# Kernel optimization log

Hardware: AMD Instinct MI355X
Metric: run time of the kernel (lower is better)

## Reference

```python
import jax, jax.numpy as jnp
import numpy as np
from jax import lax

RADIUS = 9
EPS = 1e-5
CLAMP = 100.0


def _local_corr(a_pad, b):
    """For each shift (i,j) in [0,RADIUS)^2: sum_c a_pad[:, :, i:i+h, j:j+w] * b.
    a_pad: [n,c,h+2R,w+2R] replicate-padded, b: [n,c,h,w] -> [n, R*R, h, w].
    Matches the torch loop ordering idx = i*RADIUS + j."""
    n, c, h, w = b.shape
    offs = jnp.arange(RADIUS)

    def one(i, j):
        win = lax.dynamic_slice(a_pad, (0, 0, i, j), (n, c, h, w))
        return jnp.sum(win * b, axis=1)  # [n,h,w]

    corr = jax.vmap(lambda i: jax.vmap(lambda j: one(i, j))(offs))(offs)  # [R,R,n,h,w]
    return corr.reshape(RADIUS * RADIUS, n, h, w).transpose(1, 0, 2, 3)  # [n,R*R,h,w]


def setup_inputs() -> dict:
    key = jax.random.key(0)
    k1, k2 = jax.random.split(key)
    n, c, h, w = 2, 64, 128, 192
    img = jax.random.normal(k1, (n, c, h, w), dtype=jnp.float32)
    img_map = jax.random.normal(k2, (n, c, h, w), dtype=jnp.float32)
    return {"img": img, "img_map": img_map}


def reference(img, img_map):
    # channel-wise L2 normalization (torch.norm(p=2, dim=1))
    norm_img = jnp.linalg.norm(img, axis=1, keepdims=True)
    norm_map = jnp.linalg.norm(img_map, axis=1, keepdims=True)
    img_scaled = img / (norm_img + EPS)        # torch mutates img in-place to this
    map_scaled = img_map / (norm_map + EPS)    # img_map itself NOT mutated (div, not div_)
    img_clamped = jnp.clip(img_scaled, -CLAMP, CLAMP)
    map_clamped = jnp.clip(map_scaled, -CLAMP, CLAMP)

    pad = ((0, 0), (0, 0), (RADIUS, RADIUS), (RADIUS, RADIUS))
    map_clamped_pad = jnp.pad(map_clamped, pad, mode='edge')  # F.pad 'replicate'
    map_orig_pad = jnp.pad(img_map, pad, mode='edge')

    # out_cos = 1 - <clamped normalized img, shifted clamped normalized map>
    out_cos = 1.0 - _local_corr(map_clamped_pad, img_clamped)
    # out_diss uses the in-place-normalized (UNclamped) img and the ORIGINAL img_map
    out_diss = _local_corr(map_orig_pad, img_scaled)
    return out_cos, out_diss
```

## Files before the change

kernel.cpp:

```cpp
#include <hip/hip_runtime.h>
#include <math.h>

namespace {
constexpr int RADIUS = 9;
constexpr float EPSV = 1e-5f;
constexpr int N_ = 2, C_ = 64, H_ = 128, W_ = 192;
constexpr int HW  = H_ * W_;
constexpr int CHW = C_ * HW;
constexpr size_t OUT1 = (size_t)N_ * 81 * HW;

constexpr int XT = 64, YT = 4;
constexpr int NT = 256;
constexpr int NW = 4;
constexpr int ROUNDS = 16;
constexpr int MROWS = 4;
constexpr int NCH = 19;
constexpr int MCOLS = 76;
constexpr int MAP_SLOTS = MROWS * NCH;
constexpr int OFF_INVM = 5 * 256 * 4;
constexpr int LDS_F = OFF_INVM + MROWS * MCOLS;
}

__global__ __launch_bounds__(64)
void norms_kernel(const float* __restrict__ mp,
                  float* __restrict__ invM) {
    __shared__ float4 sM[8][8];
    const int tid = threadIdx.x;
    const int cg = tid >> 3;
    const int s  = tid & 7;
    const int q4 = blockIdx.x * 8 + s;
    const int n = q4 / (HW / 4);
    const int pix = (q4 - n * (HW / 4)) * 4;
    const float* pm = mp + (size_t)n * CHW + pix;

    float4 sm = {0.f, 0.f, 0.f, 0.f};
#pragma unroll
    for (int cc = 0; cc < 8; ++cc) {
        float4 b = *(const float4*)(pm + (size_t)(cg * 8 + cc) * HW);
        sm.x = fmaf(b.x, b.x, sm.x); sm.y = fmaf(b.y, b.y, sm.y);
        sm.z = fmaf(b.z, b.z, sm.z); sm.w = fmaf(b.w, b.w, sm.w);
    }
    sM[cg][s] = sm;
    __syncthreads();
    if (tid < 8) {
        float4 b = sM[0][tid];
#pragma unroll
        for (int g = 1; g < 8; ++g) {
            float4 v = sM[g][tid];
            b.x += v.x; b.y += v.y; b.z += v.z; b.w += v.w;
        }
        float4 vm;
        vm.x = 1.f / (sqrtf(b.x) + EPSV); vm.y = 1.f / (sqrtf(b.y) + EPSV);
        vm.z = 1.f / (sqrtf(b.z) + EPSV); vm.w = 1.f / (sqrtf(b.w) + EPSV);
        *(float4*)(invM + (size_t)n * HW + pix) = vm;
    }
}

__global__ __launch_bounds__(NT)
void corr_kernel(const float* __restrict__ img,
                 const float* __restrict__ mp,
                 const float* __restrict__ invMg,
                 float* __restrict__ out) {
    __shared__ float smem[LDS_F];

    const int bz = blockIdx.z;
    const int n    = bz / RADIUS;
    const int iOff = bz - n * RADIUS;
    const int y0 = blockIdx.y * YT;
    const int x0 = blockIdx.x * XT;
    const int tid = threadIdx.x;
    const int w    = tid >> 6;
    const int lane = tid & 63;
    const int ty = lane >> 4;
    const int xc = lane & 15;
    const int ch0 = w * 16;

    const float* imgN = img + (size_t)n * CHW;
    const float* mapN = mp  + (size_t)n * CHW;

    if (tid < MAP_SLOTS) {
        int r = tid / NCH, k = tid - r * NCH;
        int gy = min(max(y0 + iOff - RADIUS + r, 0), H_ - 1);
        int gxs = x0 - 12 + 4 * k;
        const float* src = invMg + n * HW + (size_t)gy * W_;
        float4 v;
        if (gxs >= 0) v = *(const float4*)(src + gxs);
        else { float s0 = src[0]; v.x = s0; v.y = s0; v.z = s0; v.w = s0; }
        *(float4*)&smem[OFF_INVM + r * MCOLS + 4 * k] = v;
    }

    const int gy = min(max(y0 + ty + iOff - RADIUS, 0), H_ - 1);
    const float* rowp = mapN + (size_t)ch0 * HW + (size_t)gy * W_;
    bool bc[4]; const float* pd[4];
#pragma unroll
    for (int d = 0; d < 4; ++d) {
        int gx = x0 + 4 * xc - 12 + 4 * d;
        bc[d] = (gx < 0);
        pd[d] = rowp + (gx < 0 ? 0 : gx);
    }
    const float* pI = imgN + (size_t)ch0 * HW + (size_t)(y0 + ty) * W_ + x0 + 4 * xc;

    float acc[4][RADIUS];
#pragma unroll
    for (int p = 0; p < 4; ++p)
#pragma unroll
        for (int j = 0; j < RADIUS; ++j) acc[p][j] = 0.f;
    float si[4] = {0.f, 0.f, 0.f, 0.f};

#pragma unroll 4
    for (int ri = 0; ri < ROUNDS; ++ri) {
        const size_t off = (size_t)ri * HW;
        float wreg[16];
        *(float4*)&wreg[0]  = *(const float4*)(pd[0] + off);
        *(float4*)&wreg[4]  = *(const float4*)(pd[1] + off);
        *(float4*)&wreg[8]  = *(const float4*)(pd[2] + off);
        *(float4*)&wreg[12] = *(const float4*)(pd[3] + off);
        const float4 a4 = *(const float4*)(pI + off);
#pragma unroll
        for (int d = 0; d < 3; ++d) {
            if (bc[d]) { wreg[4*d+1] = wreg[4*d]; wreg[4*d+2] = wreg[4*d]; wreg[4*d+3] = wreg[4*d]; }
        }
        const float a[4] = {a4.x, a4.y, a4.z, a4.w};
        si[0] = fmaf(a[0], a[0], si[0]);
        si[1] = fmaf(a[1], a[1], si[1]);
        si[2] = fmaf(a[2], a[2], si[2]);
        si[3] = fmaf(a[3], a[3], si[3]);
#pragma unroll
        for (int p = 0; p < 4; ++p)
#pragma unroll
            for (int j = 0; j < RADIUS; ++j)
                acc[p][j] = fmaf(wreg[p + j + 3], a[p], acc[p][j]);
    }

    __syncthreads();
    const int slot = tid;
#pragma unroll
    for (int q = 0; q < 4; ++q) {
        float4 v = {acc[0][q], acc[1][q], acc[2][q], acc[3][q]};
        *(float4*)&smem[(q * 256 + slot) * 4] = v;
    }
    { float4 v = {si[0], si[1], si[2], si[3]}; *(float4*)&smem[(4 * 256 + slot) * 4] = v; }
    __syncthreads();
    float4 sv = {0.f, 0.f, 0.f, 0.f};
#pragma unroll
    for (int g = 0; g < NW; ++g) {
        float4 v = *(const float4*)&smem[(4 * 256 + g * 64 + lane) * 4];
        sv.x += v.x; sv.y += v.y; sv.z += v.z; sv.w += v.w;
    }
    float4 vI;
    vI.x = 1.f / (sqrtf(sv.x) + EPSV);
    vI.y = 1.f / (sqrtf(sv.y) + EPSV);
    vI.z = 1.f / (sqrtf(sv.z) + EPSV);
    vI.w = 1.f / (sqrtf(sv.w) + EPSV);

    const int y  = y0 + ty;
    const int xb = x0 + 4 * xc;
    const float* wmRow = &smem[OFF_INVM + ty * MCOLS + 4 * xc + 3];
    float* ocB = out + (size_t)(n * 81 + iOff * RADIUS) * HW + (size_t)y * W_ + xb;

    {
        const int j = w;
        float4 s = {0.f, 0.f, 0.f, 0.f};
#pragma unroll
        for (int g = 0; g < NW; ++g) {
            float4 v = *(const float4*)&smem[(j * 256 + g * 64 + lane) * 4];
            s.x += v.x; s.y += v.y; s.z += v.z; s.w += v.w;
        }
        float4 vd, vc;
        vd.x = s.x * vI.x; vd.y = s.y * vI.y; vd.z = s.z * vI.z; vd.w = s.w * vI.w;
        vc.x = 1.f - vd.x * wmRow[j + 0];
        vc.y = 1.f - vd.y * wmRow[j + 1];
        vc.z = 1.f - vd.z * wmRow[j + 2];
        vc.w = 1.f - vd.w * wmRow[j + 3];
        *(float4*)(ocB + (size_t)j * HW) = vc;
        *(float4*)(ocB + OUT1 + (size_t)j * HW) = vd;
    }
    __syncthreads();
#pragma unroll
    for (int q = 0; q < 5; ++q) {
        float4 v = {acc[0][q + 4], acc[1][q + 4], acc[2][q + 4], acc[3][q + 4]};
        *(float4*)&smem[(q * 256 + slot) * 4] = v;
    }
    __syncthreads();
    {
        const int j = 4 + w;
        float4 s = {0.f, 0.f, 0.f, 0.f};
#pragma unroll
        for (int g = 0; g < NW; ++g) {
            float4 v = *(const float4*)&smem[((j - 4) * 256 + g * 64 + lane) * 4];
            s.x += v.x; s.y += v.y; s.z += v.z; s.w += v.w;
        }
        float4 vd, vc;
        vd.x = s.x * vI.x; vd.y = s.y * vI.y; vd.z = s.z * vI.z; vd.w = s.w * vI.w;
        vc.x = 1.f - vd.x * wmRow[j + 0];
        vc.y = 1.f - vd.y * wmRow[j + 1];
        vc.z = 1.f - vd.z * wmRow[j + 2];
        vc.w = 1.f - vd.w * wmRow[j + 3];
        *(float4*)(ocB + (size_t)j * HW) = vc;
        *(float4*)(ocB + OUT1 + (size_t)j * HW) = vd;
    }
    if (w == 0) {
        const int j = 8;
        float4 s = {0.f, 0.f, 0.f, 0.f};
#pragma unroll
        for (int g = 0; g < NW; ++g) {
            float4 v = *(const float4*)&smem[(4 * 256 + g * 64 + lane) * 4];
            s.x += v.x; s.y += v.y; s.z += v.z; s.w += v.w;
        }
        float4 vd, vc;
        vd.x = s.x * vI.x; vd.y = s.y * vI.y; vd.z = s.z * vI.z; vd.w = s.w * vI.w;
        vc.x = 1.f - vd.x * wmRow[j + 0];
        vc.y = 1.f - vd.y * wmRow[j + 1];
        vc.z = 1.f - vd.z * wmRow[j + 2];
        vc.w = 1.f - vd.w * wmRow[j + 3];
        *(float4*)(ocB + (size_t)j * HW) = vc;
        *(float4*)(ocB + OUT1 + (size_t)j * HW) = vd;
    }
}

extern "C" void kernel_launch(void* const* d_in, const int* in_sizes, int n_in,
                              void* d_out, int out_size, void* d_ws, size_t ws_size,
                              hipStream_t stream) {
    const float* img = (const float*)d_in[0];
    const float* mp  = (const float*)d_in[1];
    float* out  = (float*)d_out;
    float* invM = (float*)d_ws;

    norms_kernel<<<(N_ * HW / 4) / 8, 64, 0, stream>>>(mp, invM);

    dim3 grid(W_ / XT, H_ / YT, N_ * RADIUS);
    corr_kernel<<<grid, NT, 0, stream>>>(img, mp, invM, out);
}
```

Baseline: 40.98 us.

## Precompute left-edge replicate strip and reorder grid so iOff varies fastest

The norms kernel now also writes a small per-channel, per-row strip holding the replicated left-edge map value as float4. The corr kernel reads from this strip for out-of-bounds left columns instead of patching registers per round, which removes the branchy register fixup from the inner loop. The grid is also reordered so the 18 (n, iOff) shift blocks for the same tile launch next to each other, which should improve L2 reuse of the shared img and map data. In exchange there are extra workspace writes and per-pointer strides in the hot loop.

```diff
diff --git a/kernel.cpp b/kernel.cpp
--- a/kernel.cpp
+++ b/kernel.cpp
@@ -23,7 +23,8 @@
 
 __global__ __launch_bounds__(64)
 void norms_kernel(const float* __restrict__ mp,
-                  float* __restrict__ invM) {
+                  float* __restrict__ invM,
+                  float* __restrict__ strip) {
     __shared__ float4 sM[8][8];
     const int tid = threadIdx.x;
     const int cg = tid >> 3;
@@ -31,7 +32,11 @@
     const int q4 = blockIdx.x * 8 + s;
     const int n = q4 / (HW / 4);
     const int pix = (q4 - n * (HW / 4)) * 4;
+    const int y = pix / W_;
+    const int x = pix - y * W_;
     const float* pm = mp + (size_t)n * CHW + pix;
+    const bool e = (x == 0);
+    float* sp = strip + ((size_t)(n * C_ + cg * 8) * H_ + y) * 4;
 
     float4 sm = {0.f, 0.f, 0.f, 0.f};
 #pragma unroll
@@ -39,6 +44,7 @@
         float4 b = *(const float4*)(pm + (size_t)(cg * 8 + cc) * HW);
         sm.x = fmaf(b.x, b.x, sm.x); sm.y = fmaf(b.y, b.y, sm.y);
         sm.z = fmaf(b.z, b.z, sm.z); sm.w = fmaf(b.w, b.w, sm.w);
+        if (e) { float4 v = {b.x, b.x, b.x, b.x}; *(float4*)(sp + (size_t)cc * H_ * 4) = v; }
     }
     sM[cg][s] = sm;
     __syncthreads();
@@ -60,14 +66,15 @@
 void corr_kernel(const float* __restrict__ img,
                  const float* __restrict__ mp,
                  const float* __restrict__ invMg,
+                 const float* __restrict__ strip,
                  float* __restrict__ out) {
     __shared__ float smem[LDS_F];
 
-    const int bz = blockIdx.z;
+    const int bz = blockIdx.x;
     const int n    = bz / RADIUS;
     const int iOff = bz - n * RADIUS;
-    const int y0 = blockIdx.y * YT;
-    const int x0 = blockIdx.x * XT;
+    const int x0 = blockIdx.y * XT;
+    const int y0 = blockIdx.z * YT;
     const int tid = threadIdx.x;
     const int w    = tid >> 6;
     const int lane = tid & 63;
@@ -91,12 +98,13 @@
 
     const int gy = min(max(y0 + ty + iOff - RADIUS, 0), H_ - 1);
     const float* rowp = mapN + (size_t)ch0 * HW + (size_t)gy * W_;
-    bool bc[4]; const float* pd[4];
+    const float* stripRow = strip + ((size_t)(n * C_ + ch0) * H_ + gy) * 4;
+    const float* pd[4]; int sd[4];
 #pragma unroll
     for (int d = 0; d < 4; ++d) {
         int gx = x0 + 4 * xc - 12 + 4 * d;
-        bc[d] = (gx < 0);
-        pd[d] = rowp + (gx < 0 ? 0 : gx);
+        if (gx < 0) { pd[d] = stripRow; sd[d] = H_ * 4; }
+        else        { pd[d] = rowp + gx; sd[d] = HW; }
     }
     const float* pI = imgN + (size_t)ch0 * HW + (size_t)(y0 + ty) * W_ + x0 + 4 * xc;
 
@@ -109,17 +117,12 @@
 
 #pragma unroll 4
     for (int ri = 0; ri < ROUNDS; ++ri) {
-        const size_t off = (size_t)ri * HW;
         float wreg[16];
-        *(float4*)&wreg[0]  = *(const float4*)(pd[0] + off);
-        *(float4*)&wreg[4]  = *(const float4*)(pd[1] + off);
-        *(float4*)&wreg[8]  = *(const float4*)(pd[2] + off);
-        *(float4*)&wreg[12] = *(const float4*)(pd[3] + off);
-        const float4 a4 = *(const float4*)(pI + off);
-#pragma unroll
-        for (int d = 0; d < 3; ++d) {
-            if (bc[d]) { wreg[4*d+1] = wreg[4*d]; wreg[4*d+2] = wreg[4*d]; wreg[4*d+3] = wreg[4*d]; }
-        }
+        *(float4*)&wreg[0]  = *(const float4*)(pd[0] + (size_t)ri * sd[0]);
+        *(float4*)&wreg[4]  = *(const float4*)(pd[1] + (size_t)ri * sd[1]);
+        *(float4*)&wreg[8]  = *(const float4*)(pd[2] + (size_t)ri * sd[2]);
+        *(float4*)&wreg[12] = *(const float4*)(pd[3] + (size_t)ri * sd[3]);
+        const float4 a4 = *(const float4*)(pI + (size_t)ri * HW);
         const float a[4] = {a4.x, a4.y, a4.z, a4.w};
         si[0] = fmaf(a[0], a[0], si[0]);
         si[1] = fmaf(a[1], a[1], si[1]);
@@ -223,11 +226,12 @@
                               hipStream_t stream) {
     const float* img = (const float*)d_in[0];
     const float* mp  = (const float*)d_in[1];
-    float* out  = (float*)d_out;
-    float* invM = (float*)d_ws;
-
-    norms_kernel<<<(N_ * HW / 4) / 8, 64, 0, stream>>>(mp, invM);
-
-    dim3 grid(W_ / XT, H_ / YT, N_ * RADIUS);
-    corr_kernel<<<grid, NT, 0, stream>>>(img, mp, invM, out);
-}
+    float* out   = (float*)d_out;
+    float* invM  = (float*)d_ws;
+    float* strip = invM + N_ * HW;
+
+    norms_kernel<<<(N_ * HW / 4) / 8, 64, 0, stream>>>(mp, invM, strip);
+
+    dim3 grid(N_ * RADIUS, W_ / XT, H_ / YT);
+    corr_kernel<<<grid, NT, 0, stream>>>(img, mp, invM, strip, out);
+}
```

After: 45.16 us. 1.1x slower.

## Precompute replicate-padded edge strips and load three unaligned map vectors per channel

Applied to the files above, without the earlier changes.

The norms kernel grows to 256 threads per block and also writes two small per-channel, per-row strips holding left-edge replicate-padded values. The correlation kernel then reads exactly 12 map floats per channel through three possibly unaligned 16-byte loads instead of four aligned loads plus per-lane edge fixups. For left-edge lanes the loads are redirected to the strips with their own stride. This cuts map load traffic and removes the clamping selects from the inner loop. In exchange it adds extra strip writes in the first kernel and relies on unaligned vector global loads.

```diff
diff --git a/kernel.cpp b/kernel.cpp
--- a/kernel.cpp
+++ b/kernel.cpp
@@ -21,38 +21,54 @@
 constexpr int LDS_F = OFF_INVM + MROWS * MCOLS;
 }
 
-__global__ __launch_bounds__(64)
+__global__ __launch_bounds__(256)
 void norms_kernel(const float* __restrict__ mp,
-                  float* __restrict__ invM) {
-    __shared__ float4 sM[8][8];
+                  float* __restrict__ invM,
+                  float* __restrict__ strip,
+                  float* __restrict__ strip2) {
+    __shared__ float4 sM[8][32];
     const int tid = threadIdx.x;
-    const int cg = tid >> 3;
-    const int s  = tid & 7;
-    const int q4 = blockIdx.x * 8 + s;
+    const int cg = tid >> 5;
+    const int s  = tid & 31;
+    const int q4 = blockIdx.x * 32 + s;
     const int n = q4 / (HW / 4);
     const int pix = (q4 - n * (HW / 4)) * 4;
+    const int y = pix / W_;
+    const int x = pix - y * W_;
     const float* pm = mp + (size_t)n * CHW + pix;
+    const bool e = (x == 0);
+    float* sp  = strip  + ((size_t)(n * C_ + cg * 8) * H_ + y) * 4;
+    float* sp2 = strip2 + ((size_t)(n * C_ + cg * 8) * H_ + y) * 4;
 
     float4 sm = {0.f, 0.f, 0.f, 0.f};
 #pragma unroll
     for (int cc = 0; cc < 8; ++cc) {
-        float4 b = *(const float4*)(pm + (size_t)(cg * 8 + cc) * HW);
+        float4 b = *(const float4*)(pm + (size_t)(cc + 0) * HW + (size_t)cg * 8 * HW);
         sm.x = fmaf(b.x, b.x, sm.x); sm.y = fmaf(b.y, b.y, sm.y);
         sm.z = fmaf(b.z, b.z, sm.z); sm.w = fmaf(b.w, b.w, sm.w);
+        if (e) {
+            float4 v1 = {b.x, b.x, b.x, b.x};
+            float4 v2 = {b.x, b.x, b.y, b.z};
+            *(float4*)(sp  + (size_t)cc * H_ * 4) = v1;
+            *(float4*)(sp2 + (size_t)cc * H_ * 4) = v2;
+        }
     }
     sM[cg][s] = sm;
     __syncthreads();
-    if (tid < 8) {
+    if (tid < 32) {
         float4 b = sM[0][tid];
 #pragma unroll
         for (int g = 1; g < 8; ++g) {
             float4 v = sM[g][tid];
             b.x += v.x; b.y += v.y; b.z += v.z; b.w += v.w;
         }
+        int q4b = blockIdx.x * 32 + tid;
+        int nb = q4b / (HW / 4);
+        int pixb = (q4b - nb * (HW / 4)) * 4;
         float4 vm;
         vm.x = 1.f / (sqrtf(b.x) + EPSV); vm.y = 1.f / (sqrtf(b.y) + EPSV);
         vm.z = 1.f / (sqrtf(b.z) + EPSV); vm.w = 1.f / (sqrtf(b.w) + EPSV);
-        *(float4*)(invM + (size_t)n * HW + pix) = vm;
+        *(float4*)(invM + (size_t)nb * HW + pixb) = vm;
     }
 }
 
@@ -60,14 +76,16 @@
 void corr_kernel(const float* __restrict__ img,
                  const float* __restrict__ mp,
                  const float* __restrict__ invMg,
+                 const float* __restrict__ strip,
+                 const float* __restrict__ strip2,
                  float* __restrict__ out) {
     __shared__ float smem[LDS_F];
 
     const int bz = blockIdx.z;
     const int n    = bz / RADIUS;
     const int iOff = bz - n * RADIUS;
+    const int x0 = blockIdx.x * XT;
     const int y0 = blockIdx.y * YT;
-    const int x0 = blockIdx.x * XT;
     const int tid = threadIdx.x;
     const int w    = tid >> 6;
     const int lane = tid & 63;
@@ -91,12 +109,22 @@
 
     const int gy = min(max(y0 + ty + iOff - RADIUS, 0), H_ - 1);
     const float* rowp = mapN + (size_t)ch0 * HW + (size_t)gy * W_;
-    bool bc[4]; const float* pd[4];
-#pragma unroll
-    for (int d = 0; d < 4; ++d) {
-        int gx = x0 + 4 * xc - 12 + 4 * d;
-        bc[d] = (gx < 0);
-        pd[d] = rowp + (gx < 0 ? 0 : gx);
+    const float* stripRow  = strip  + ((size_t)(n * C_ + ch0) * H_ + gy) * 4;
+    const float* stripRow2 = strip2 + ((size_t)(n * C_ + ch0) * H_ + gy) * 4;
+    const float *pd0, *pd1, *pd2;
+    int sd0, sd1, sd2;
+    {
+        const int gxb = x0 + 4 * xc - 9;
+        if (gxb <= -4)     { pd0 = stripRow;  sd0 = H_ * 4; }
+        else if (gxb < 0)  { pd0 = stripRow2; sd0 = H_ * 4; }
+        else               { pd0 = rowp + gxb; sd0 = HW; }
+        const int g1 = gxb + 4;
+        if (g1 <= -4)      { pd1 = stripRow;  sd1 = H_ * 4; }
+        else if (g1 < 0)   { pd1 = stripRow2; sd1 = H_ * 4; }
+        else               { pd1 = rowp + g1;  sd1 = HW; }
+        const int g2 = gxb + 8;
+        if (g2 < 0)        { pd2 = stripRow2; sd2 = H_ * 4; }
+        else               { pd2 = rowp + g2;  sd2 = HW; }
     }
     const float* pI = imgN + (size_t)ch0 * HW + (size_t)(y0 + ty) * W_ + x0 + 4 * xc;
 
@@ -109,17 +137,11 @@
 
 #pragma unroll 4
     for (int ri = 0; ri < ROUNDS; ++ri) {
-        const size_t off = (size_t)ri * HW;
-        float wreg[16];
-        *(float4*)&wreg[0]  = *(const float4*)(pd[0] + off);
-        *(float4*)&wreg[4]  = *(const float4*)(pd[1] + off);
-        *(float4*)&wreg[8]  = *(const float4*)(pd[2] + off);
-        *(float4*)&wreg[12] = *(const float4*)(pd[3] + off);
-        const float4 a4 = *(const float4*)(pI + off);
-#pragma unroll
-        for (int d = 0; d < 3; ++d) {
-            if (bc[d]) { wreg[4*d+1] = wreg[4*d]; wreg[4*d+2] = wreg[4*d]; wreg[4*d+3] = wreg[4*d]; }
-        }
+        float wreg[12];
+        __builtin_memcpy(&wreg[0], pd0 + (size_t)ri * sd0, 16);
+        __builtin_memcpy(&wreg[4], pd1 + (size_t)ri * sd1, 16);
+        __builtin_memcpy(&wreg[8], pd2 + (size_t)ri * sd2, 16);
+        const float4 a4 = *(const float4*)(pI + (size_t)ri * HW);
         const float a[4] = {a4.x, a4.y, a4.z, a4.w};
         si[0] = fmaf(a[0], a[0], si[0]);
         si[1] = fmaf(a[1], a[1], si[1]);
@@ -129,7 +151,7 @@
         for (int p = 0; p < 4; ++p)
 #pragma unroll
             for (int j = 0; j < RADIUS; ++j)
-                acc[p][j] = fmaf(wreg[p + j + 3], a[p], acc[p][j]);
+                acc[p][j] = fmaf(wreg[p + j], a[p], acc[p][j]);
     }
 
     __syncthreads();
@@ -223,11 +245,13 @@
                               hipStream_t stream) {
     const float* img = (const float*)d_in[0];
     const float* mp  = (const float*)d_in[1];
-    float* out  = (float*)d_out;
-    float* invM = (float*)d_ws;
-
-    norms_kernel<<<(N_ * HW / 4) / 8, 64, 0, stream>>>(mp, invM);
+    float* out    = (float*)d_out;
+    float* invM   = (float*)d_ws;
+    float* strip  = invM  + N_ * HW;
+    float* strip2 = strip + (size_t)N_ * C_ * H_ * 4;
+
+    norms_kernel<<<(N_ * HW / 4) / 32, 256, 0, stream>>>(mp, invM, strip, strip2);
 
     dim3 grid(W_ / XT, H_ / YT, N_ * RADIUS);
-    corr_kernel<<<grid, NT, 0, stream>>>(img, mp, invM, out);
-}
+    corr_kernel<<<grid, NT, 0, stream>>>(img, mp, invM, strip, strip2, out);
+}
```

Measured after the change: 33.04 us (median of 3 runs). -19.4%, faster.

## Pre-normalize img and convert inputs to bf16 in a fused prepass kernel

Applied to the files above, without the earlier changes.

The norms kernel now computes both image and map channel norms, writes a normalized image and the raw map as bf16 copies, and builds a small padded left-edge strip buffer for replicate padding. The correlation kernel reads these bf16 arrays, which halves its global traffic, and no longer computes or reduces the image norm. The cost is an extra full read and write pass in the prepass, plus bf16 rounding of inputs that may exceed accuracy tolerance.

```diff
diff --git a/kernel.cpp b/kernel.cpp
--- a/kernel.cpp
+++ b/kernel.cpp
@@ -19,64 +19,115 @@
 constexpr int MAP_SLOTS = MROWS * NCH;
 constexpr int OFF_INVM = 5 * 256 * 4;
 constexpr int LDS_F = OFF_INVM + MROWS * MCOLS;
-}
-
-__global__ __launch_bounds__(64)
-void norms_kernel(const float* __restrict__ mp,
-                  float* __restrict__ invM) {
-    __shared__ float4 sM[8][8];
+constexpr int SW = 32;
+}
+
+__device__ __forceinline__ unsigned short f2bf(float f) {
+    unsigned u = __float_as_uint(f);
+    unsigned r = ((u >> 16) & 1u) + 0x7fffu;
+    return (unsigned short)((u + r) >> 16);
+}
+__device__ __forceinline__ float bflo(unsigned d) { return __uint_as_float(d << 16); }
+__device__ __forceinline__ float bfhi(unsigned d) { return __uint_as_float(d & 0xffff0000u); }
+
+__global__ __launch_bounds__(256)
+void norms_kernel(const float* __restrict__ img,
+                  const float* __restrict__ mp,
+                  float* __restrict__ invM,
+                  unsigned short* __restrict__ imgs,
+                  unsigned short* __restrict__ mapb,
+                  unsigned short* __restrict__ stripB) {
+    __shared__ float4 sI[8][32], sM[8][32];
     const int tid = threadIdx.x;
-    const int cg = tid >> 3;
-    const int s  = tid & 7;
-    const int q4 = blockIdx.x * 8 + s;
+    const int cg = tid >> 5;
+    const int s  = tid & 31;
+    const int q4 = blockIdx.x * 32 + s;
     const int n = q4 / (HW / 4);
     const int pix = (q4 - n * (HW / 4)) * 4;
-    const float* pm = mp + (size_t)n * CHW + pix;
-
-    float4 sm = {0.f, 0.f, 0.f, 0.f};
+    const int y = pix / W_;
+    const int x = pix - y * W_;
+    const float* pi = img + (size_t)n * CHW + pix;
+    const float* pm = mp  + (size_t)n * CHW + pix;
+    const bool e = (x == 0);
+
+    float4 iv[8], mv[8];
+    float4 si = {0.f, 0.f, 0.f, 0.f}, sm = {0.f, 0.f, 0.f, 0.f};
 #pragma unroll
     for (int cc = 0; cc < 8; ++cc) {
-        float4 b = *(const float4*)(pm + (size_t)(cg * 8 + cc) * HW);
-        sm.x = fmaf(b.x, b.x, sm.x); sm.y = fmaf(b.y, b.y, sm.y);
-        sm.z = fmaf(b.z, b.z, sm.z); sm.w = fmaf(b.w, b.w, sm.w);
-    }
-    sM[cg][s] = sm;
-    __syncthreads();
-    if (tid < 8) {
-        float4 b = sM[0][tid];
-#pragma unroll
-        for (int g = 1; g < 8; ++g) {
-            float4 v = sM[g][tid];
-            b.x += v.x; b.y += v.y; b.z += v.z; b.w += v.w;
-        }
+        iv[cc] = *(const float4*)(pi + (size_t)(cg * 8 + cc) * HW);
+        mv[cc] = *(const float4*)(pm + (size_t)(cg * 8 + cc) * HW);
+        si.x = fmaf(iv[cc].x, iv[cc].x, si.x); si.y = fmaf(iv[cc].y, iv[cc].y, si.y);
+        si.z = fmaf(iv[cc].z, iv[cc].z, si.z); si.w = fmaf(iv[cc].w, iv[cc].w, si.w);
+        sm.x = fmaf(mv[cc].x, mv[cc].x, sm.x); sm.y = fmaf(mv[cc].y, mv[cc].y, sm.y);
+        sm.z = fmaf(mv[cc].z, mv[cc].z, sm.z); sm.w = fmaf(mv[cc].w, mv[cc].w, sm.w);
+    }
+    sI[cg][s] = si; sM[cg][s] = sm;
+    __syncthreads();
+    float4 ti = {0.f, 0.f, 0.f, 0.f}, tm = {0.f, 0.f, 0.f, 0.f};
+#pragma unroll
+    for (int g = 0; g < 8; ++g) {
+        float4 a = sI[g][s], b = sM[g][s];
+        ti.x += a.x; ti.y += a.y; ti.z += a.z; ti.w += a.w;
+        tm.x += b.x; tm.y += b.y; tm.z += b.z; tm.w += b.w;
+    }
+    float4 vi;
+    vi.x = 1.f / (sqrtf(ti.x) + EPSV); vi.y = 1.f / (sqrtf(ti.y) + EPSV);
+    vi.z = 1.f / (sqrtf(ti.z) + EPSV); vi.w = 1.f / (sqrtf(ti.w) + EPSV);
+    if (cg == 0) {
         float4 vm;
-        vm.x = 1.f / (sqrtf(b.x) + EPSV); vm.y = 1.f / (sqrtf(b.y) + EPSV);
-        vm.z = 1.f / (sqrtf(b.z) + EPSV); vm.w = 1.f / (sqrtf(b.w) + EPSV);
+        vm.x = 1.f / (sqrtf(tm.x) + EPSV); vm.y = 1.f / (sqrtf(tm.y) + EPSV);
+        vm.z = 1.f / (sqrtf(tm.z) + EPSV); vm.w = 1.f / (sqrtf(tm.w) + EPSV);
         *(float4*)(invM + (size_t)n * HW + pix) = vm;
     }
+    unsigned short* ib = imgs + (size_t)n * CHW + pix;
+    unsigned short* mb = mapb + (size_t)n * CHW + pix;
+#pragma unroll
+    for (int cc = 0; cc < 8; ++cc) {
+        const size_t o = (size_t)(cg * 8 + cc) * HW;
+        ushort4 a4;
+        a4.x = f2bf(iv[cc].x * vi.x); a4.y = f2bf(iv[cc].y * vi.y);
+        a4.z = f2bf(iv[cc].z * vi.z); a4.w = f2bf(iv[cc].w * vi.w);
+        *(ushort4*)(ib + o) = a4;
+        ushort4 b4;
+        b4.x = f2bf(mv[cc].x); b4.y = f2bf(mv[cc].y);
+        b4.z = f2bf(mv[cc].z); b4.w = f2bf(mv[cc].w);
+        *(ushort4*)(mb + o) = b4;
+        if (e) {
+            const float* mrow = pm + o;
+            unsigned short b0 = b4.x, b1 = b4.y;
+            unsigned short bb2 = b4.z, bb3 = b4.w;
+            unsigned short bb4 = f2bf(mrow[4]), bb5 = f2bf(mrow[5]);
+            unsigned short* sr = stripB + ((size_t)(n * C_ + cg * 8 + cc) * H_ + y) * SW;
+            ushort4 q0 = {b0, b0, b0, b0};
+            ushort4 q1 = {b0, b0, b0, b1};
+            ushort4 q2 = {bb2, bb3, bb4, bb5};
+            *(ushort4*)(sr + 0)  = q0; *(ushort4*)(sr + 4)  = q0;
+            *(ushort4*)(sr + 8)  = q0; *(ushort4*)(sr + 12) = q1;
+            *(ushort4*)(sr + 16) = q1; *(ushort4*)(sr + 20) = q2;
+            *(ushort4*)(sr + 24) = q1;
+        }
+    }
 }
 
 __global__ __launch_bounds__(NT)
-void corr_kernel(const float* __restrict__ img,
-                 const float* __restrict__ mp,
+void corr_kernel(const unsigned short* __restrict__ imgs,
+                 const unsigned short* __restrict__ mapb,
                  const float* __restrict__ invMg,
+                 const unsigned short* __restrict__ stripB,
                  float* __restrict__ out) {
     __shared__ float smem[LDS_F];
 
     const int bz = blockIdx.z;
     const int n    = bz / RADIUS;
     const int iOff = bz - n * RADIUS;
+    const int x0 = blockIdx.x * XT;
     const int y0 = blockIdx.y * YT;
-    const int x0 = blockIdx.x * XT;
     const int tid = threadIdx.x;
     const int w    = tid >> 6;
     const int lane = tid & 63;
     const int ty = lane >> 4;
     const int xc = lane & 15;
     const int ch0 = w * 16;
-
-    const float* imgN = img + (size_t)n * CHW;
-    const float* mapN = mp  + (size_t)n * CHW;
 
     if (tid < MAP_SLOTS) {
         int r = tid / NCH, k = tid - r * NCH;
@@ -90,74 +141,63 @@
     }
 
     const int gy = min(max(y0 + ty + iOff - RADIUS, 0), H_ - 1);
-    const float* rowp = mapN + (size_t)ch0 * HW + (size_t)gy * W_;
-    bool bc[4]; const float* pd[4];
-#pragma unroll
-    for (int d = 0; d < 4; ++d) {
-        int gx = x0 + 4 * xc - 12 + 4 * d;
-        bc[d] = (gx < 0);
-        pd[d] = rowp + (gx < 0 ? 0 : gx);
-    }
-    const float* pI = imgN + (size_t)ch0 * HW + (size_t)(y0 + ty) * W_ + x0 + 4 * xc;
+    const unsigned short* rowb = mapb + (size_t)n * CHW + (size_t)ch0 * HW
+                               + (size_t)gy * W_;
+    const unsigned short* srow = stripB + ((size_t)(n * C_ + ch0) * H_ + gy) * SW;
+    const unsigned short *pA, *pB2, *pC;
+    int sA, sB, sC;
+    {
+        const int e0 = x0 + 4 * xc - 10;
+        if (e0 <= -8)      { pA = srow + 0;  sA = H_ * SW; }
+        else if (e0 <= -4) { pA = srow + 8;  sA = H_ * SW; }
+        else if (e0 < 0)   { pA = srow + 16; sA = H_ * SW; }
+        else               { pA = rowb + e0; sA = HW; }
+        const int eB = e0 + 8;
+        if (eB < 0)        { pB2 = srow + 24; sB = H_ * SW; }
+        else               { pB2 = rowb + eB; sB = HW; }
+        pC = rowb + e0 + 12; sC = HW;
+    }
+    const unsigned short* pI2 = imgs + (size_t)n * CHW + (size_t)ch0 * HW
+                              + (size_t)(y0 + ty) * W_ + x0 + 4 * xc;
 
     float acc[4][RADIUS];
 #pragma unroll
     for (int p = 0; p < 4; ++p)
 #pragma unroll
         for (int j = 0; j < RADIUS; ++j) acc[p][j] = 0.f;
-    float si[4] = {0.f, 0.f, 0.f, 0.f};
 
 #pragma unroll 4
     for (int ri = 0; ri < ROUNDS; ++ri) {
-        const size_t off = (size_t)ri * HW;
-        float wreg[16];
-        *(float4*)&wreg[0]  = *(const float4*)(pd[0] + off);
-        *(float4*)&wreg[4]  = *(const float4*)(pd[1] + off);
-        *(float4*)&wreg[8]  = *(const float4*)(pd[2] + off);
-        *(float4*)&wreg[12] = *(const float4*)(pd[3] + off);
-        const float4 a4 = *(const float4*)(pI + off);
-#pragma unroll
-        for (int d = 0; d < 3; ++d) {
-            if (bc[d]) { wreg[4*d+1] = wreg[4*d]; wreg[4*d+2] = wreg[4*d]; wreg[4*d+3] = wreg[4*d]; }
-        }
-        const float a[4] = {a4.x, a4.y, a4.z, a4.w};
-        si[0] = fmaf(a[0], a[0], si[0]);
-        si[1] = fmaf(a[1], a[1], si[1]);
-        si[2] = fmaf(a[2], a[2], si[2]);
-        si[3] = fmaf(a[3], a[3], si[3]);
+        unsigned dA[4]; __builtin_memcpy(dA, pA  + (size_t)ri * sA, 16);
+        unsigned dB[2]; __builtin_memcpy(dB, pB2 + (size_t)ri * sB, 8);
+        unsigned dC;    __builtin_memcpy(&dC, pC + (size_t)ri * sC, 4);
+        unsigned dI[2]; __builtin_memcpy(dI, pI2 + (size_t)ri * HW, 8);
+        float wv[12];
+        wv[0]  = bfhi(dA[0]); wv[1]  = bflo(dA[1]); wv[2]  = bfhi(dA[1]);
+        wv[3]  = bflo(dA[2]); wv[4]  = bfhi(dA[2]); wv[5]  = bflo(dA[3]);
+        wv[6]  = bfhi(dA[3]); wv[7]  = bflo(dB[0]); wv[8]  = bfhi(dB[0]);
+        wv[9]  = bflo(dB[1]); wv[10] = bfhi(dB[1]); wv[11] = bflo(dC);
+        const float a[4] = {bflo(dI[0]), bfhi(dI[0]), bflo(dI[1]), bfhi(dI[1])};
 #pragma unroll
         for (int p = 0; p < 4; ++p)
 #pragma unroll
             for (int j = 0; j < RADIUS; ++j)
-                acc[p][j] = fmaf(wreg[p + j + 3], a[p], acc[p][j]);
+                acc[p][j] = fmaf(wv[p + j], a[p], acc[p][j]);
     }
 
     __syncthreads();
     const int slot = tid;
-#pragma unroll
-    for (int q = 0; q < 4; ++q) {
-        float4 v = {acc[0][q], acc[1][q], acc[2][q], acc[3][q]};
-        *(float4*)&smem[(q * 256 + slot) * 4] = v;
-    }
-    { float4 v = {si[0], si[1], si[2], si[3]}; *(float4*)&smem[(4 * 256 + slot) * 4] = v; }
-    __syncthreads();
-    float4 sv = {0.f, 0.f, 0.f, 0.f};
-#pragma unroll
-    for (int g = 0; g < NW; ++g) {
-        float4 v = *(const float4*)&smem[(4 * 256 + g * 64 + lane) * 4];
-        sv.x += v.x; sv.y += v.y; sv.z += v.z; sv.w += v.w;
-    }
-    float4 vI;
-    vI.x = 1.f / (sqrtf(sv.x) + EPSV);
-    vI.y = 1.f / (sqrtf(sv.y) + EPSV);
-    vI.z = 1.f / (sqrtf(sv.z) + EPSV);
-    vI.w = 1.f / (sqrtf(sv.w) + EPSV);
-
     const int y  = y0 + ty;
     const int xb = x0 + 4 * xc;
     const float* wmRow = &smem[OFF_INVM + ty * MCOLS + 4 * xc + 3];
     float* ocB = out + (size_t)(n * 81 + iOff * RADIUS) * HW + (size_t)y * W_ + xb;
 
+#pragma unroll
+    for (int q = 0; q < 4; ++q) {
+        float4 v = {acc[0][q], acc[1][q], acc[2][q], acc[3][q]};
+        *(float4*)&smem[(q * 256 + slot) * 4] = v;
+    }
+    __syncthreads();
     {
         const int j = w;
         float4 s = {0.f, 0.f, 0.f, 0.f};
@@ -166,14 +206,13 @@
             float4 v = *(const float4*)&smem[(j * 256 + g * 64 + lane) * 4];
             s.x += v.x; s.y += v.y; s.z += v.z; s.w += v.w;
         }
-        float4 vd, vc;
-        vd.x = s.x * vI.x; vd.y = s.y * vI.y; vd.z = s.z * vI.z; vd.w = s.w * vI.w;
-        vc.x = 1.f - vd.x * wmRow[j + 0];
-        vc.y = 1.f - vd.y * wmRow[j + 1];
-        vc.z = 1.f - vd.z * wmRow[j + 2];
-        vc.w = 1.f - vd.w * wmRow[j + 3];
+        float4 vc;
+        vc.x = 1.f - s.x * wmRow[j + 0];
+        vc.y = 1.f - s.y * wmRow[j + 1];
+        vc.z = 1.f - s.z * wmRow[j + 2];
+        vc.w = 1.f - s.w * wmRow[j + 3];
         *(float4*)(ocB + (size_t)j * HW) = vc;
-        *(float4*)(ocB + OUT1 + (size_t)j * HW) = vd;
+        *(float4*)(ocB + OUT1 + (size_t)j * HW) = s;
     }
     __syncthreads();
 #pragma unroll
@@ -190,14 +229,13 @@
             float4 v = *(const float4*)&smem[((j - 4) * 256 + g * 64 + lane) * 4];
             s.x += v.x; s.y += v.y; s.z += v.z; s.w += v.w;
         }
-        float4 vd, vc;
-        vd.x = s.x * vI.x; vd.y = s.y * vI.y; vd.z = s.z * vI.z; vd.w = s.w * vI.w;
-        vc.x = 1.f - vd.x * wmRow[j + 0];
-        vc.y = 1.f - vd.y * wmRow[j + 1];
-        vc.z = 1.f - vd.z * wmRow[j + 2];
-        vc.w = 1.f - vd.w * wmRow[j + 3];
+        float4 vc;
+        vc.x = 1.f - s.x * wmRow[j + 0];
+        vc.y = 1.f - s.y * wmRow[j + 1];
+        vc.z = 1.f - s.z * wmRow[j + 2];
+        vc.w = 1.f - s.w * wmRow[j + 3];
         *(float4*)(ocB + (size_t)j * HW) = vc;
-        *(float4*)(ocB + OUT1 + (size_t)j * HW) = vd;
+        *(float4*)(ocB + OUT1 + (size_t)j * HW) = s;
     }
     if (w == 0) {
         const int j = 8;
@@ -207,14 +245,13 @@
             float4 v = *(const float4*)&smem[(4 * 256 + g * 64 + lane) * 4];
             s.x += v.x; s.y += v.y; s.z += v.z; s.w += v.w;
         }
-        float4 vd, vc;
-        vd.x = s.x * vI.x; vd.y = s.y * vI.y; vd.z = s.z * vI.z; vd.w = s.w * vI.w;
-        vc.x = 1.f - vd.x * wmRow[j + 0];
-        vc.y = 1.f - vd.y * wmRow[j + 1];
-        vc.z = 1.f - vd.z * wmRow[j + 2];
-        vc.w = 1.f - vd.w * wmRow[j + 3];
+        float4 vc;
+        vc.x = 1.f - s.x * wmRow[j + 0];
+        vc.y = 1.f - s.y * wmRow[j + 1];
+        vc.z = 1.f - s.z * wmRow[j + 2];
+        vc.w = 1.f - s.w * wmRow[j + 3];
         *(float4*)(ocB + (size_t)j * HW) = vc;
-        *(float4*)(ocB + OUT1 + (size_t)j * HW) = vd;
+        *(float4*)(ocB + OUT1 + (size_t)j * HW) = s;
     }
 }
 
@@ -223,11 +260,15 @@
                               hipStream_t stream) {
     const float* img = (const float*)d_in[0];
     const float* mp  = (const float*)d_in[1];
-    float* out  = (float*)d_out;
+    float* out = (float*)d_out;
     float* invM = (float*)d_ws;
-
-    norms_kernel<<<(N_ * HW / 4) / 8, 64, 0, stream>>>(mp, invM);
+    unsigned short* stripB = (unsigned short*)((char*)d_ws + 196608);
+    unsigned short* imgs   = (unsigned short*)((char*)d_ws + 196608 + 1048576);
+    unsigned short* mapb   = imgs + (size_t)N_ * CHW;
+
+    norms_kernel<<<(N_ * HW / 4) / 32, 256, 0, stream>>>(img, mp, invM,
+                                                         imgs, mapb, stripB);
 
     dim3 grid(W_ / XT, H_ / YT, N_ * RADIUS);
-    corr_kernel<<<grid, NT, 0, stream>>>(img, mp, invM, out);
-}
+    corr_kernel<<<grid, NT, 0, stream>>>(imgs, mapb, invM, stripB, out);
+}
```

After: 44.32 us. 8.1% more time.
